# Kernel tuning notes

Hardware: AMD Instinct MI355X
Metric: run time of the kernel (lower is better)

## Reference

```python
import jax, jax.numpy as jnp
import numpy as np

LAMBDA_D = 250.0
POS_MARGIN = 1.0
NEG_MARGIN = 0.2
BLOCK = 8          # block_size in the original
DIST_THRESH = 7.5  # correspondence threshold in pixels
EPS = 1e-12        # F.normalize eps


def _l2_normalize(x, axis):
    # matches torch.nn.functional.normalize: x / max(||x||_2, eps)
    n = jnp.linalg.norm(x, axis=axis, keepdims=True)
    return x / jnp.maximum(n, EPS)


def setup_inputs() -> dict:
    key = jax.random.key(0)
    k1, k2, k3 = jax.random.split(key, 3)
    b, d, hc, wc = 2, 256, 60, 80  # 480x640 image, block 8
    desc = jax.random.normal(k1, (b, d, hc, wc), dtype=jnp.float32)
    wrap_desc = jax.random.normal(k2, (b, d, hc, wc), dtype=jnp.float32)
    # realistic near-identity homographies (random H would warp everything off-image)
    H = jnp.eye(3, dtype=jnp.float32)[None] + 0.02 * jax.random.normal(k3, (b, 3, 3), dtype=jnp.float32)
    return {"desc": desc, "wrap_desc": wrap_desc, "H": H}


def reference(desc, wrap_desc, H):
    b, d, hc, wc = desc.shape
    n = hc * wc

    # cell-center coordinates in (row, col) order, shape (hc, wc, 2)
    coords = jnp.stack(
        jnp.meshgrid(jnp.arange(hc), jnp.arange(wc), indexing="ij"), axis=-1
    ).astype(jnp.float32) * BLOCK + BLOCK // 2

    # homogeneous (x, y, 1) points, shape (n, 3)
    xy1 = jnp.concatenate(
        [coords[..., 1:2], coords[..., 0:1], jnp.ones((hc, wc, 1), jnp.float32)],
        axis=-1,
    ).reshape(n, 3)

    # warp by homography: (b, n, 3)
    w = jnp.einsum("bij,nj->bni", H, xy1)
    wxy = w[..., :2] / w[..., 2:3]                       # (b, n, 2) in (x, y)
    warp = jnp.stack([wxy[..., 1], wxy[..., 0]], axis=-1).reshape(b, hc, wc, 2)  # (row, col)

    # distance between warped query centers and all cell centers: (b, hc, wc, hc, wc)
    dist = jnp.linalg.norm(coords[None, None, None] - warp[:, :, :, None, None, :], axis=-1)
    S = (dist <= DIST_THRESH).astype(desc.dtype)

    # unit-normalized descriptors, channel-last
    dn = _l2_normalize(jnp.transpose(desc, (0, 2, 3, 1)), axis=-1)       # (b, hc, wc, d)
    wn = _l2_normalize(jnp.transpose(wrap_desc, (0, 2, 3, 1)), axis=-1)  # (b, hc, wc, d)

    # full correlation volume via batched GEMM (same math as broadcast-sum)
    dot = jax.nn.relu(jnp.einsum("bijd,bkld->bijkl", dn, wn))           # (b,hc,wc,hc,wc)

    # normalize over warped-cell axis (k, l), then over query-cell axis (i, j)
    dot = _l2_normalize(dot.reshape(b, hc, wc, n), axis=3).reshape(b, hc, wc, hc, wc)
    dot = _l2_normalize(dot.reshape(b, n, hc, wc), axis=1).reshape(b, hc, wc, hc, wc)

    loss = LAMBDA_D * S * jax.nn.relu(POS_MARGIN - dot) + (1.0 - S) * jax.nn.relu(dot - NEG_MARGIN)
    # sum over (i,j,k,l) per image / n^2, then sum over batch == total sum / n^2
    return jnp.sum(loss) / float(n * n)
```

## Files before the change

### kernel.cpp

```cpp
#include <hip/hip_runtime.h>

#define HC 60
#define WCC 80
#define NCELL 4800
#define NP 4864
#define NB 38
#define DCH 256
#define BATCH 2
#define QT 64

typedef _Float16 half8 __attribute__((ext_vector_type(8)));
typedef float f32x4 __attribute__((ext_vector_type(4)));

__device__ __forceinline__ void gload_lds16(const void* gp, void* lp) {
  __builtin_amdgcn_global_load_lds(
      (const __attribute__((address_space(1))) void*)gp,
      (__attribute__((address_space(3))) void*)lp, 16, 0, 0);
}

__global__ __launch_bounds__(256) void warp_kernel(const float* __restrict__ H,
                                                   float* __restrict__ wout) {
  int idx = blockIdx.x * 256 + threadIdx.x;
  if (idx >= BATCH * NP) return;
  int b = idx / NP;
  int q = idx - b * NP;
  float wr = 1e9f, wc = 1e9f;
  if (q < NCELL) {
    int i = q / WCC;
    int j = q - i * WCC;
    float x = (float)(j * 8 + 4);
    float y = (float)(i * 8 + 4);
    const float* h = H + b * 9;
    float w0 = h[0] * x + h[1] * y + h[2];
    float w1 = h[3] * x + h[4] * y + h[5];
    float w2 = h[6] * x + h[7] * y + h[8];
    wr = w1 / w2;
    wc = w0 / w2;
  }
  wout[2 * idx]     = wr;
  wout[2 * idx + 1] = wc;
}

__global__ __launch_bounds__(256) void normalize_kernel(
    const float* __restrict__ desc, const float* __restrict__ wdesc,
    _Float16* __restrict__ dnp, _Float16* __restrict__ wnp) {
  __shared__ _Float16 vt[DCH][QT + 2];
  __shared__ float pss[4][QT];
  __shared__ float invq[QT];
  const int q0 = blockIdx.x * QT;
  const int which = blockIdx.y;
  const int b = blockIdx.z;
  const float* in = which ? wdesc : desc;
  _Float16* out = which ? wnp : dnp;
  const int tx = threadIdx.x & 63;
  const int ty = threadIdx.x >> 6;
  const int q = q0 + tx;
  float ss = 0.f;
  for (int cc = 0; cc < DCH / 4; ++cc) {
    const int c = cc * 4 + ty;
    float v = (q < NCELL) ? in[((size_t)b * DCH + c) * NCELL + q] : 0.f;
    vt[c][tx] = (_Float16)v;
    ss += v * v;
  }
  pss[ty][tx] = ss;
  __syncthreads();
  if (ty == 0) {
    float tot = pss[0][tx] + pss[1][tx] + pss[2][tx] + pss[3][tx];
    invq[tx] = 1.f / fmaxf(sqrtf(tot), 1e-12f);
  }
  __syncthreads();
  for (int it = 0; it < QT; ++it) {
    out[((size_t)b * NP + q0 + it) * DCH + threadIdx.x] =
        (_Float16)((float)vt[threadIdx.x][it] * invq[it]);
  }
}

template <int MODE>
__global__ __launch_bounds__(256) void gemm_kernel(
    const _Float16* __restrict__ A, const _Float16* __restrict__ Bm,
    const float* __restrict__ invr, const float* __restrict__ colscale,
    const float* __restrict__ warp, float* __restrict__ sqacc,
    float* __restrict__ lossp) {
  __shared__ _Float16 As[128][64];
  __shared__ _Float16 Bs[128][64];
  const int tid = threadIdx.x;
  const int wave = tid >> 6;
  const int lane = tid & 63;
  const int batch = blockIdx.z;
  const int row0 = blockIdx.y * 128;
  const int col0 = blockIdx.x * 128;
  const _Float16* Ab = A + ((size_t)batch * NP + row0) * DCH;
  const _Float16* Bb = Bm + ((size_t)batch * NP + col0) * DCH;

  const int wq_r = wave >> 1;
  const int wq_c = wave & 1;
  const int g = lane >> 4;
  const int cL = lane & 15;

  f32x4 acc[4][4] = {};

  const int srow = lane >> 3;
  const int scol = lane & 7;
  const int sc_swz = (scol ^ srow) * 8;

  for (int ks = 0; ks < 4; ++ks) {
#pragma unroll
    for (int c = 0; c < 4; ++c) {
      const int chunk = wave * 4 + c;
      const int r = chunk * 8 + srow;
      gload_lds16(Ab + (size_t)r * DCH + ks * 64 + sc_swz,
                  (char*)(&As[0][0]) + chunk * 1024);
      gload_lds16(Bb + (size_t)r * DCH + ks * 64 + sc_swz,
                  (char*)(&Bs[0][0]) + chunk * 1024);
    }
    __syncthreads();
#pragma unroll
    for (int kk = 0; kk < 2; ++kk) {
      half8 af[4], bf[4];
#pragma unroll
      for (int m = 0; m < 4; ++m) {
        const int row = wq_r * 64 + m * 16 + cL;
        const int c16 = (kk * 4 + g) ^ (row & 7);
        af[m] = *reinterpret_cast<const half8*>(
            (const char*)(&As[0][0]) + row * 128 + c16 * 16);
      }
#pragma unroll
      for (int n = 0; n < 4; ++n) {
        const int row = wq_c * 64 + n * 16 + cL;
        const int c16 = (kk * 4 + g) ^ (row & 7);
        bf[n] = *reinterpret_cast<const half8*>(
            (const char*)(&Bs[0][0]) + row * 128 + c16 * 16);
      }
#pragma unroll
      for (int m = 0; m < 4; ++m)
#pragma unroll
        for (int n = 0; n < 4; ++n)
          acc[m][n] =
              __builtin_amdgcn_mfma_f32_16x16x32_f16(af[m], bf[n], acc[m][n], 0, 0, 0);
    }
    __syncthreads();
  }

  if (MODE == 0 || MODE == 1) {
    float cs[4];
    if (MODE == 1) {
#pragma unroll
      for (int n = 0; n < 4; ++n)
        cs[n] = colscale[(size_t)batch * NP + col0 + wq_c * 64 + n * 16 + cL];
    }
    float rs[4][4];
#pragma unroll
    for (int m = 0; m < 4; ++m)
#pragma unroll
      for (int j = 0; j < 4; ++j) rs[m][j] = 0.f;
#pragma unroll
    for (int m = 0; m < 4; ++m)
#pragma unroll
      for (int n = 0; n < 4; ++n)
#pragma unroll
        for (int j = 0; j < 4; ++j) {
          float u = fmaxf(acc[m][n][j], 0.f);
          if (MODE == 1) u *= cs[n];
          rs[m][j] += u * u;
        }
#pragma unroll
    for (int m = 0; m < 4; ++m)
#pragma unroll
      for (int j = 0; j < 4; ++j) {
        float v = rs[m][j];
        v += __shfl_xor(v, 1, 64);
        v += __shfl_xor(v, 2, 64);
        v += __shfl_xor(v, 4, 64);
        v += __shfl_xor(v, 8, 64);
        if (cL == 0)
          atomicAdd(&sqacc[(size_t)batch * NP + row0 + wq_r * 64 + m * 16 + g * 4 + j], v);
      }
  } else {
    float cy[4], cx[4], ic[4];
    int cvalid[4];
#pragma unroll
    for (int n = 0; n < 4; ++n) {
      int ct = col0 + wq_c * 64 + n * 16 + cL;
      cvalid[n] = (ct < NCELL);
      int tk = ct / WCC;
      int tl = ct - tk * WCC;
      cy[n] = (float)(tk * 8 + 4);
      cx[n] = (float)(tl * 8 + 4);
      ic[n] = colscale[(size_t)batch * NP + ct];
    }
    float lsum = 0.f;
#pragma unroll
    for (int m = 0; m < 4; ++m)
#pragma unroll
      for (int j = 0; j < 4; ++j) {
        const int rq = row0 + wq_r * 64 + m * 16 + g * 4 + j;
        if (rq < NCELL) {
          const float ir = invr[(size_t)batch * NP + rq];
          const float wr = warp[((size_t)batch * NP + rq) * 2];
          const float wcol = warp[((size_t)batch * NP + rq) * 2 + 1];
#pragma unroll
          for (int n = 0; n < 4; ++n) {
            if (cvalid[n]) {
              float u = fmaxf(acc[m][n][j], 0.f);
              float v = u * ir * ic[n];
              float dr = cy[n] - wr;
              float dc = cx[n] - wcol;
              float pos = 250.f * fmaxf(1.f - v, 0.f);
              float neg = fmaxf(v - 0.2f, 0.f);
              lsum += (dr * dr + dc * dc <= 56.25f) ? pos : neg;
            }
          }
        }
      }
#pragma unroll
    for (int s = 1; s < 64; s <<= 1) lsum += __shfl_xor(lsum, s, 64);
    if (lane == 0) {
      int slot = (((batch * NB + blockIdx.y) * NB + blockIdx.x) << 2) | wave;
      lossp[slot] = lsum;
    }
  }
}

__global__ void finalize_inv(const float* __restrict__ sq, float* __restrict__ inv,
                             int count) {
  int i = blockIdx.x * 256 + threadIdx.x;
  if (i < count) inv[i] = 1.f / fmaxf(sqrtf(sq[i]), 1e-12f);
}

__global__ __launch_bounds__(1024) void loss_reduce(const float* __restrict__ lossp,
                                                    float* __restrict__ out) {
  const int COUNT = BATCH * NB * NB * 4;
  double s = 0.0;
  for (int i = threadIdx.x; i < COUNT; i += 1024) s += (double)lossp[i];
#pragma unroll
  for (int k = 1; k < 64; k <<= 1) s += __shfl_xor(s, k, 64);
  __shared__ double sd[16];
  if ((threadIdx.x & 63) == 0) sd[threadIdx.x >> 6] = s;
  __syncthreads();
  if (threadIdx.x == 0) {
    double t = 0.0;
    for (int w = 0; w < 16; ++w) t += sd[w];
    out[0] = (float)(t / ((double)NCELL * (double)NCELL));
  }
}

extern "C" void kernel_launch(void* const* d_in, const int* in_sizes, int n_in,
                              void* d_out, int out_size, void* d_ws, size_t ws_size,
                              hipStream_t stream) {
  const float* desc  = (const float*)d_in[0];
  const float* wdesc = (const float*)d_in[1];
  const float* H     = (const float*)d_in[2];
  char* ws = (char*)d_ws;

  constexpr size_t SZ_HALF = (size_t)BATCH * NP * DCH * sizeof(_Float16);
  constexpr size_t SZ_WARP = (size_t)BATCH * NP * 2 * sizeof(float);
  constexpr size_t SZ_VEC  = (size_t)BATCH * NP * sizeof(float);
  constexpr size_t SZ_LOSS = (size_t)BATCH * NB * NB * 4 * sizeof(float);
  constexpr size_t OFF_DNP  = 0;
  constexpr size_t OFF_WNP  = OFF_DNP + SZ_HALF;
  constexpr size_t OFF_WARP = OFF_WNP + SZ_HALF;
  constexpr size_t OFF_R2   = OFF_WARP + SZ_WARP;
  constexpr size_t OFF_INVR = OFF_R2 + SZ_VEC;
  constexpr size_t OFF_C2   = OFF_INVR + SZ_VEC;
  constexpr size_t OFF_INVC = OFF_C2 + SZ_VEC;
  constexpr size_t OFF_LOSS = OFF_INVC + SZ_VEC;

  _Float16* dnp = (_Float16*)(ws + OFF_DNP);
  _Float16* wnp = (_Float16*)(ws + OFF_WNP);
  float* warp = (float*)(ws + OFF_WARP);
  float* r2   = (float*)(ws + OFF_R2);
  float* invr = (float*)(ws + OFF_INVR);
  float* c2   = (float*)(ws + OFF_C2);
  float* invc = (float*)(ws + OFF_INVC);
  float* lossp = (float*)(ws + OFF_LOSS);

  hipMemsetAsync(r2, 0, SZ_VEC, stream);
  hipMemsetAsync(c2, 0, SZ_VEC, stream);

  warp_kernel<<<dim3((BATCH * NP + 255) / 256), 256, 0, stream>>>(H, warp);
  normalize_kernel<<<dim3(NP / QT, 2, BATCH), 256, 0, stream>>>(desc, wdesc, dnp, wnp);

  dim3 gg(NB, NB, BATCH);
  gemm_kernel<0><<<gg, 256, 0, stream>>>(dnp, wnp, nullptr, nullptr, nullptr, r2, nullptr);
  finalize_inv<<<(BATCH * NP + 255) / 256, 256, 0, stream>>>(r2, invr, BATCH * NP);
  gemm_kernel<1><<<gg, 256, 0, stream>>>(wnp, dnp, nullptr, invr, nullptr, c2, nullptr);
  finalize_inv<<<(BATCH * NP + 255) / 256, 256, 0, stream>>>(c2, invc, BATCH * NP);
  gemm_kernel<2><<<gg, 256, 0, stream>>>(dnp, wnp, invr, invc, warp, nullptr, lossp);
  loss_reduce<<<1, 1024, 0, stream>>>(lossp, (float*)d_out);
}
```

Before: 250.5 us.

## Widen GEMM K-tile to 128, fold inverse-norm finalize into GEMM epilogues

The GEMM now stages 128-wide K slices in shared memory, so each tile runs two load/sync rounds instead of four, and the XOR swizzle moves to 16 units. Launch bounds now request two blocks per CU. The separate finalize_inv kernels are removed, and each consumer computes 1/max(sqrt(sumsq), eps) inline from the accumulated squared sums. The two memsets are merged into one. This cuts kernel launches and barriers, but doubles LDS per block to 64KB, which may limit occupancy, and repeats some sqrt/reciprocal work in the epilogues.

```diff
diff --git a/kernel.cpp b/kernel.cpp
--- a/kernel.cpp
+++ b/kernel.cpp
@@ -76,13 +76,13 @@
 }
 
 template <int MODE>
-__global__ __launch_bounds__(256) void gemm_kernel(
+__global__ __launch_bounds__(256, 2) void gemm_kernel(
     const _Float16* __restrict__ A, const _Float16* __restrict__ Bm,
-    const float* __restrict__ invr, const float* __restrict__ colscale,
+    const float* __restrict__ rowsq, const float* __restrict__ colsq,
     const float* __restrict__ warp, float* __restrict__ sqacc,
     float* __restrict__ lossp) {
-  __shared__ _Float16 As[128][64];
-  __shared__ _Float16 Bs[128][64];
+  __shared__ _Float16 As[128][128];
+  __shared__ _Float16 Bs[128][128];
   const int tid = threadIdx.x;
   const int wave = tid >> 6;
   const int lane = tid & 63;
@@ -99,37 +99,37 @@
 
   f32x4 acc[4][4] = {};
 
-  const int srow = lane >> 3;
-  const int scol = lane & 7;
-  const int sc_swz = (scol ^ srow) * 8;
-
-  for (int ks = 0; ks < 4; ++ks) {
-#pragma unroll
-    for (int c = 0; c < 4; ++c) {
-      const int chunk = wave * 4 + c;
-      const int r = chunk * 8 + srow;
-      gload_lds16(Ab + (size_t)r * DCH + ks * 64 + sc_swz,
+  const int srow4 = lane >> 4;
+  const int sunit = lane & 15;
+
+  for (int ks = 0; ks < 2; ++ks) {
+#pragma unroll
+    for (int c = 0; c < 8; ++c) {
+      const int chunk = wave * 8 + c;
+      const int r = chunk * 4 + srow4;
+      const int gcol = ks * 128 + ((sunit ^ (r & 15)) << 3);
+      gload_lds16(Ab + (size_t)r * DCH + gcol,
                   (char*)(&As[0][0]) + chunk * 1024);
-      gload_lds16(Bb + (size_t)r * DCH + ks * 64 + sc_swz,
+      gload_lds16(Bb + (size_t)r * DCH + gcol,
                   (char*)(&Bs[0][0]) + chunk * 1024);
     }
     __syncthreads();
 #pragma unroll
-    for (int kk = 0; kk < 2; ++kk) {
+    for (int kk = 0; kk < 4; ++kk) {
       half8 af[4], bf[4];
 #pragma unroll
       for (int m = 0; m < 4; ++m) {
         const int row = wq_r * 64 + m * 16 + cL;
-        const int c16 = (kk * 4 + g) ^ (row & 7);
+        const int u16 = (kk * 4 + g) ^ (row & 15);
         af[m] = *reinterpret_cast<const half8*>(
-            (const char*)(&As[0][0]) + row * 128 + c16 * 16);
+            (const char*)(&As[0][0]) + row * 256 + u16 * 16);
       }
 #pragma unroll
       for (int n = 0; n < 4; ++n) {
         const int row = wq_c * 64 + n * 16 + cL;
-        const int c16 = (kk * 4 + g) ^ (row & 7);
+        const int u16 = (kk * 4 + g) ^ (row & 15);
         bf[n] = *reinterpret_cast<const half8*>(
-            (const char*)(&Bs[0][0]) + row * 128 + c16 * 16);
+            (const char*)(&Bs[0][0]) + row * 256 + u16 * 16);
       }
 #pragma unroll
       for (int m = 0; m < 4; ++m)
@@ -145,8 +145,10 @@
     float cs[4];
     if (MODE == 1) {
 #pragma unroll
-      for (int n = 0; n < 4; ++n)
-        cs[n] = colscale[(size_t)batch * NP + col0 + wq_c * 64 + n * 16 + cL];
+      for (int n = 0; n < 4; ++n) {
+        float v = colsq[(size_t)batch * NP + col0 + wq_c * 64 + n * 16 + cL];
+        cs[n] = 1.f / fmaxf(sqrtf(v), 1e-12f);
+      }
     }
     float rs[4][4];
 #pragma unroll
@@ -186,7 +188,7 @@
       int tl = ct - tk * WCC;
       cy[n] = (float)(tk * 8 + 4);
       cx[n] = (float)(tl * 8 + 4);
-      ic[n] = colscale[(size_t)batch * NP + ct];
+      ic[n] = 1.f / fmaxf(sqrtf(colsq[(size_t)batch * NP + ct]), 1e-12f);
     }
     float lsum = 0.f;
 #pragma unroll
@@ -195,15 +197,16 @@
       for (int j = 0; j < 4; ++j) {
         const int rq = row0 + wq_r * 64 + m * 16 + g * 4 + j;
         if (rq < NCELL) {
-          const float ir = invr[(size_t)batch * NP + rq];
-          const float wr = warp[((size_t)batch * NP + rq) * 2];
+          const float ir =
+              1.f / fmaxf(sqrtf(rowsq[(size_t)batch * NP + rq]), 1e-12f);
+          const float wrr = warp[((size_t)batch * NP + rq) * 2];
           const float wcol = warp[((size_t)batch * NP + rq) * 2 + 1];
 #pragma unroll
           for (int n = 0; n < 4; ++n) {
             if (cvalid[n]) {
               float u = fmaxf(acc[m][n][j], 0.f);
               float v = u * ir * ic[n];
-              float dr = cy[n] - wr;
+              float dr = cy[n] - wrr;
               float dc = cx[n] - wcol;
               float pos = 250.f * fmaxf(1.f - v, 0.f);
               float neg = fmaxf(v - 0.2f, 0.f);
@@ -221,17 +224,10 @@
   }
 }
 
-__global__ void finalize_inv(const float* __restrict__ sq, float* __restrict__ inv,
-                             int count) {
-  int i = blockIdx.x * 256 + threadIdx.x;
-  if (i < count) inv[i] = 1.f / fmaxf(sqrtf(sq[i]), 1e-12f);
-}
-
 __global__ __launch_bounds__(1024) void loss_reduce(const float* __restrict__ lossp,
-                                                    float* __restrict__ out) {
-  const int COUNT = BATCH * NB * NB * 4;
+                                                    float* __restrict__ out, int count) {
   double s = 0.0;
-  for (int i = threadIdx.x; i < COUNT; i += 1024) s += (double)lossp[i];
+  for (int i = threadIdx.x; i < count; i += 1024) s += (double)lossp[i];
 #pragma unroll
   for (int k = 1; k < 64; k <<= 1) s += __shfl_xor(s, k, 64);
   __shared__ double sd[16];
@@ -255,36 +251,28 @@
   constexpr size_t SZ_HALF = (size_t)BATCH * NP * DCH * sizeof(_Float16);
   constexpr size_t SZ_WARP = (size_t)BATCH * NP * 2 * sizeof(float);
   constexpr size_t SZ_VEC  = (size_t)BATCH * NP * sizeof(float);
-  constexpr size_t SZ_LOSS = (size_t)BATCH * NB * NB * 4 * sizeof(float);
   constexpr size_t OFF_DNP  = 0;
   constexpr size_t OFF_WNP  = OFF_DNP + SZ_HALF;
   constexpr size_t OFF_WARP = OFF_WNP + SZ_HALF;
   constexpr size_t OFF_R2   = OFF_WARP + SZ_WARP;
-  constexpr size_t OFF_INVR = OFF_R2 + SZ_VEC;
-  constexpr size_t OFF_C2   = OFF_INVR + SZ_VEC;
-  constexpr size_t OFF_INVC = OFF_C2 + SZ_VEC;
-  constexpr size_t OFF_LOSS = OFF_INVC + SZ_VEC;
+  constexpr size_t OFF_C2   = OFF_R2 + SZ_VEC;
+  constexpr size_t OFF_LOSS = OFF_C2 + SZ_VEC;
 
   _Float16* dnp = (_Float16*)(ws + OFF_DNP);
   _Float16* wnp = (_Float16*)(ws + OFF_WNP);
   float* warp = (float*)(ws + OFF_WARP);
   float* r2   = (float*)(ws + OFF_R2);
-  float* invr = (float*)(ws + OFF_INVR);
   float* c2   = (float*)(ws + OFF_C2);
-  float* invc = (float*)(ws + OFF_INVC);
   float* lossp = (float*)(ws + OFF_LOSS);
 
-  hipMemsetAsync(r2, 0, SZ_VEC, stream);
-  hipMemsetAsync(c2, 0, SZ_VEC, stream);
+  hipMemsetAsync(r2, 0, 2 * SZ_VEC, stream);
 
   warp_kernel<<<dim3((BATCH * NP + 255) / 256), 256, 0, stream>>>(H, warp);
   normalize_kernel<<<dim3(NP / QT, 2, BATCH), 256, 0, stream>>>(desc, wdesc, dnp, wnp);
 
   dim3 gg(NB, NB, BATCH);
   gemm_kernel<0><<<gg, 256, 0, stream>>>(dnp, wnp, nullptr, nullptr, nullptr, r2, nullptr);
-  finalize_inv<<<(BATCH * NP + 255) / 256, 256, 0, stream>>>(r2, invr, BATCH * NP);
-  gemm_kernel<1><<<gg, 256, 0, stream>>>(wnp, dnp, nullptr, invr, nullptr, c2, nullptr);
-  finalize_inv<<<(BATCH * NP + 255) / 256, 256, 0, stream>>>(c2, invc, BATCH * NP);
-  gemm_kernel<2><<<gg, 256, 0, stream>>>(dnp, wnp, invr, invc, warp, nullptr, lossp);
-  loss_reduce<<<1, 1024, 0, stream>>>(lossp, (float*)d_out);
-}
+  gemm_kernel<1><<<gg, 256, 0, stream>>>(wnp, dnp, nullptr, r2, nullptr, c2, nullptr);
+  gemm_kernel<2><<<gg, 256, 0, stream>>>(dnp, wnp, r2, c2, warp, nullptr, lossp);
+  loss_reduce<<<1, 1024, 0, stream>>>(lossp, (float*)d_out, BATCH * NB * NB * 4);
+}
```

Result: slower. 300.0 us (+19.8%).
